# Optimization experiments

Hardware: AMD Instinct MI355X
Metric: run time of the kernel (lower is better)

Reference implementation:

```python
import jax, jax.numpy as jnp
import numpy as np

N, H, S, R, T = 32768, 512, 8, 64, 12

def setup_inputs() -> dict:
    key = jax.random.key(0)
    ks = jax.random.split(key, 7)
    scale = 1.0 / np.sqrt(H)
    return {
        "encodings": jax.random.normal(ks[0], (N, H), dtype=jnp.float32),
        "domain_encs": jax.random.normal(ks[1], (S, H), dtype=jnp.float32),
        "Us": jax.random.normal(ks[2], (S, H, R), dtype=jnp.float32) * scale,
        "W1": jax.random.normal(ks[3], (S, H, H), dtype=jnp.float32) * scale,
        "b1": jax.random.normal(ks[4], (S, H), dtype=jnp.float32) * 0.01,
        "W2": jax.random.normal(ks[5], (S, H, T), dtype=jnp.float32) * scale,
        "b2": jax.random.normal(ks[6], (S, T), dtype=jnp.float32) * 0.01,
    }

def reference(encodings, domain_encs, Us, W1, b1, W2, b2):
    # Mahalanobis soft routing. Original computes (p-mu) @ (U U^T) @ (p-mu)^T
    # and takes sqrt(diag) -- algebraically identical to project-then-square-sum.
    diff = encodings[None, :, :] - domain_encs[:, None, :]        # [S, N, H]
    proj = jnp.einsum('snh,shr->snr', diff, Us)                   # [S, N, R]
    dist = jnp.sqrt(jnp.sum(proj * proj, axis=-1))                # [S, N]
    alphas = jax.nn.softmax(-dist, axis=0)                        # softmax over sources

    # Per-source classifier: Dropout(eval=identity) -> ReLU -> Linear(H,H)
    # -> Dropout -> ReLU -> Linear(H,T) -> Sigmoid
    h0 = jax.nn.relu(encodings)                                   # [N, H]
    h1 = jax.nn.relu(jnp.einsum('nh,shk->snk', h0, W1) + b1[:, None, :])  # [S, N, H]
    out = jax.nn.sigmoid(jnp.einsum('snk,skt->snt', h1, W2) + b2[:, None, :])  # [S, N, T]

    # Softmax-weighted combine of expert outputs
    return jnp.sum(alphas[:, :, None] * out, axis=0)              # [N, T]
```

## Files before the change

kernel.cpp:

```cpp
#include <hip/hip_runtime.h>
#include <hip/hip_bf16.h>

typedef unsigned short u16;
typedef __bf16 bf16x8 __attribute__((ext_vector_type(8)));
typedef float f32x4 __attribute__((ext_vector_type(4)));

#define NROWS 32768
#define H 512
#define NS 8
#define NR 64
#define NT 12

#define WS_W1T   0
#define WS_UCT   4194304
#define WS_W2T   4718592
#define WS_CVEC  4849664
#define WS_ALPH  4851712

union BFU { __bf16 h; u16 u; };
__device__ __forceinline__ u16 f2bf(float v) { BFU b; b.h = (__bf16)v; return b.u; }

__device__ __forceinline__ void gload16(const u16* g, u16* l) {
  __builtin_amdgcn_global_load_lds(
      (const __attribute__((address_space(1))) unsigned int*)g,
      (__attribute__((address_space(3))) unsigned int*)l, 16, 0, 0);
}

__global__ __launch_bounds__(256) void transpose_cast(const float* __restrict__ in,
    u16* __restrict__ out, int Rr, int Cc, int Cpad) {
  __shared__ float tile[32][33];
  int b = blockIdx.z, r0 = blockIdx.x * 32, c0 = blockIdx.y * 32;
  int tx = threadIdx.x, ty = threadIdx.y;
#pragma unroll
  for (int i = 0; i < 4; i++) {
    int r = r0 + ty + i * 8, c = c0 + tx;
    float v = 0.f;
    if (r < Rr && c < Cc) v = in[((size_t)b * Rr + r) * Cc + c];
    tile[ty + i * 8][tx] = v;
  }
  __syncthreads();
#pragma unroll
  for (int i = 0; i < 4; i++) {
    int c = c0 + ty + i * 8, r = r0 + tx;
    if (c < Cpad && r < Rr) out[((size_t)b * Cpad + c) * Rr + r] = f2bf(tile[tx][ty + i * 8]);
  }
}

__global__ __launch_bounds__(64) void compute_c(const float* __restrict__ mu,
                                                const float* __restrict__ Us,
                                                float* __restrict__ cvec) {
  int s = blockIdx.x >> 6, r = blockIdx.x & 63, t = threadIdx.x;
  float acc = 0.f;
#pragma unroll
  for (int k = t; k < H; k += 64) acc += mu[s * H + k] * Us[((size_t)s * H + k) * NR + r];
#pragma unroll
  for (int m = 32; m; m >>= 1) acc += __shfl_xor(acc, m, 64);
  if (t == 0) cvec[blockIdx.x] = acc;
}

__device__ __forceinline__ void stage32r(const u16* __restrict__ g, u16* l, int wave, int lane) {
#pragma unroll
  for (int i = 0; i < 8; i++) {
    int r = wave * 8 + i;
    gload16(g + (size_t)r * 512 + (size_t)((lane ^ (r & 7)) * 8), l + r * 512);
  }
}

__global__ __launch_bounds__(256, 2) void routing(
    const float* __restrict__ enc, const u16* __restrict__ UcatT,
    const float* __restrict__ cvec, float* __restrict__ alphT) {
  __shared__ __align__(16) u16 Wst[2][32 * 512];
  __shared__ float distS[NS][64];

  const int tid = threadIdx.x;
  const int wave = tid >> 6, lane = tid & 63;
  const int lnm = lane & 15, lnq = lane >> 4;
  const int row0 = blockIdx.x * 64;

  bf16x8 afrag[16];
  {
    const float* rp = enc + (size_t)(row0 + wave * 16 + lnm) * H + lnq * 8;
#pragma unroll
    for (int ks = 0; ks < 16; ks++) {
      float4 x0 = *(const float4*)(rp + ks * 32);
      float4 x1 = *(const float4*)(rp + ks * 32 + 4);
      bf16x8 a;
      a[0] = (__bf16)x0.x; a[1] = (__bf16)x0.y; a[2] = (__bf16)x0.z; a[3] = (__bf16)x0.w;
      a[4] = (__bf16)x1.x; a[5] = (__bf16)x1.y; a[6] = (__bf16)x1.z; a[7] = (__bf16)x1.w;
      afrag[ks] = a;
    }
  }

  stage32r(UcatT, Wst[0], wave, lane);
  float dsq[4] = {0.f, 0.f, 0.f, 0.f};
#pragma unroll 1
  for (int q = 0; q < 16; q++) {
    int s = q >> 1, half = q & 1;
    __syncthreads();
    if (q < 15) stage32r(UcatT + (size_t)(q + 1) * 32 * 512, Wst[(q + 1) & 1], wave, lane);
    const u16* buf = Wst[q & 1];
    f32x4 acc[2] = {};
#pragma unroll
    for (int ks = 0; ks < 16; ks++) {
      int uu = ((ks * 4 + lnq) ^ (lnm & 7)) * 8;
      bf16x8 b0 = *(const bf16x8*)&buf[lnm * 512 + uu];
      bf16x8 b1v = *(const bf16x8*)&buf[(16 + lnm) * 512 + uu];
      acc[0] = __builtin_amdgcn_mfma_f32_16x16x32_bf16(afrag[ks], b0, acc[0], 0, 0, 0);
      acc[1] = __builtin_amdgcn_mfma_f32_16x16x32_bf16(afrag[ks], b1v, acc[1], 0, 0, 0);
    }
#pragma unroll
    for (int ct = 0; ct < 2; ct++) {
      float cv = cvec[s * 64 + half * 32 + ct * 16 + lnm];
#pragma unroll
      for (int g = 0; g < 4; g++) { float d = acc[ct][g] - cv; dsq[g] += d * d; }
    }
    if (half == 1) {
#pragma unroll
      for (int m = 1; m < 16; m <<= 1) {
#pragma unroll
        for (int g = 0; g < 4; g++) dsq[g] += __shfl_xor(dsq[g], m, 16);
      }
      if (lnm == 0) {
#pragma unroll
        for (int g = 0; g < 4; g++) distS[s][wave * 16 + lnq * 4 + g] = sqrtf(dsq[g]);
      }
#pragma unroll
      for (int g = 0; g < 4; g++) dsq[g] = 0.f;
    }
  }
  __syncthreads();
  if (tid < 64) {
    float dmin = distS[0][tid];
#pragma unroll
    for (int s = 1; s < NS; s++) dmin = fminf(dmin, distS[s][tid]);
    float den = 0.f, e[NS];
#pragma unroll
    for (int s = 0; s < NS; s++) { e[s] = __expf(dmin - distS[s][tid]); den += e[s]; }
    float inv = 1.f / den;
#pragma unroll
    for (int s = 0; s < NS; s++) alphT[(size_t)s * NROWS + row0 + tid] = e[s] * inv;
  }
}

#define H1STR 40

__device__ __forceinline__ void stageW16(const u16* __restrict__ g, u16* l, int tid) {
#pragma unroll
  for (int i = 0; i < 4; i++) {
    int flat = tid + i * 256;
    int r = flat >> 5, u = flat & 31;
    gload16(g + (size_t)r * 512 + (u ^ (r & 7)) * 8, l + flat * 8);
  }
}

__device__ __forceinline__ const u16* chunk_base(const u16* W1g, int q) {
  return W1g + ((size_t)(q >> 5) * 512 + ((q >> 1) & 15) * 32) * 512 + (q & 1) * 256;
}

__global__ __launch_bounds__(256, 2) void moe_main(
    const float* __restrict__ enc, const u16* __restrict__ W1T,
    const u16* __restrict__ W2T, const float* __restrict__ alphT,
    const float* __restrict__ b1g, const float* __restrict__ b2g,
    float* __restrict__ out) {
  __shared__ __align__(16) u16 Wst[3][32 * 256];
  __shared__ __align__(16) u16 h1c[128 * H1STR];
  __shared__ float alphS[4][128];

  const int tid = threadIdx.x;
  const int wave = tid >> 6, lane = tid & 63;
  const int lnm = lane & 15, lnq = lane >> 4;
  const int rb = blockIdx.x >> 1, sg = blockIdx.x & 1;
  const int row0 = rb * 128, sbase = sg * 4;

#pragma unroll
  for (int i = 0; i < 2; i++) {
    int u = tid + i * 256, j = u >> 7, r = u & 127;
    alphS[j][r] = alphT[(size_t)(sbase + j) * NROWS + row0 + r];
  }

  bf16x8 efrag[2][16];
#pragma unroll
  for (int t = 0; t < 2; t++) {
    const float* rp = enc + (size_t)(row0 + wave * 32 + t * 16 + lnm) * H + lnq * 8;
#pragma unroll
    for (int ks = 0; ks < 16; ks++) {
      float4 x0 = *(const float4*)(rp + ks * 32);
      float4 x1 = *(const float4*)(rp + ks * 32 + 4);
      bf16x8 a;
      a[0] = (__bf16)fmaxf(x0.x, 0.f); a[1] = (__bf16)fmaxf(x0.y, 0.f);
      a[2] = (__bf16)fmaxf(x0.z, 0.f); a[3] = (__bf16)fmaxf(x0.w, 0.f);
      a[4] = (__bf16)fmaxf(x1.x, 0.f); a[5] = (__bf16)fmaxf(x1.y, 0.f);
      a[6] = (__bf16)fmaxf(x1.z, 0.f); a[7] = (__bf16)fmaxf(x1.w, 0.f);
      efrag[t][ks] = a;
    }
  }

  __syncthreads();

  const u16* W1g = W1T + (size_t)sbase * 512 * 512;
  stageW16(chunk_base(W1g, 0), Wst[0], tid);
  int cb = 0;
  f32x4 acc[2][2];
  float fin[2][4] = {};
#pragma unroll 1
  for (int j = 0; j < 4; j++) {
    const int s = sbase + j;
    f32x4 oacc[2] = {};
#pragma unroll 1
    for (int wc = 0; wc < 16; wc++) {
      const int q = j * 32 + wc * 2;
      {
        const int nb = (cb == 2) ? 0 : cb + 1;
        stageW16(chunk_base(W1g, q + 1), Wst[nb], tid);
        asm volatile("s_waitcnt vmcnt(4)" ::: "memory");
        __builtin_amdgcn_s_barrier();
        const u16* buf = Wst[cb];
#pragma unroll
        for (int t = 0; t < 2; t++) { acc[t][0] = (f32x4){0,0,0,0}; acc[t][1] = (f32x4){0,0,0,0}; }
        __builtin_amdgcn_s_setprio(1);
#pragma unroll
        for (int ks = 0; ks < 8; ks++) {
          const int uu = ((ks * 4 + lnq) ^ (lnm & 7)) * 8;
          bf16x8 w0 = *(const bf16x8*)&buf[lnm * 256 + uu];
          bf16x8 w1 = *(const bf16x8*)&buf[(16 + lnm) * 256 + uu];
#pragma unroll
          for (int t = 0; t < 2; t++) {
            acc[t][0] = __builtin_amdgcn_mfma_f32_16x16x32_bf16(w0, efrag[t][ks], acc[t][0], 0, 0, 0);
            acc[t][1] = __builtin_amdgcn_mfma_f32_16x16x32_bf16(w1, efrag[t][ks], acc[t][1], 0, 0, 0);
          }
        }
        __builtin_amdgcn_s_setprio(0);
        cb = nb;
      }
      {
        const int nb = (cb == 2) ? 0 : cb + 1;
        if (q + 2 < 128) {
          stageW16(chunk_base(W1g, q + 2), Wst[nb], tid);
          asm volatile("s_waitcnt vmcnt(4)" ::: "memory");
        } else {
          asm volatile("s_waitcnt vmcnt(0)" ::: "memory");
        }
        __builtin_amdgcn_s_barrier();
        const u16* buf = Wst[cb];
        __builtin_amdgcn_s_setprio(1);
#pragma unroll
        for (int ks = 0; ks < 8; ks++) {
          const int uu = ((ks * 4 + lnq) ^ (lnm & 7)) * 8;
          bf16x8 w0 = *(const bf16x8*)&buf[lnm * 256 + uu];
          bf16x8 w1 = *(const bf16x8*)&buf[(16 + lnm) * 256 + uu];
#pragma unroll
          for (int t = 0; t < 2; t++) {
            acc[t][0] = __builtin_amdgcn_mfma_f32_16x16x32_bf16(w0, efrag[t][8 + ks], acc[t][0], 0, 0, 0);
            acc[t][1] = __builtin_amdgcn_mfma_f32_16x16x32_bf16(w1, efrag[t][8 + ks], acc[t][1], 0, 0, 0);
          }
        }
        __builtin_amdgcn_s_setprio(0);
        cb = nb;
      }
#pragma unroll
      for (int ct = 0; ct < 2; ct++) {
        float4 bq = *(const float4*)&b1g[s * H + wc * 32 + ct * 16 + lnq * 4];
#pragma unroll
        for (int t = 0; t < 2; t++) {
          union { u16 u[4]; uint2 v; } pk;
          pk.u[0] = f2bf(fmaxf(acc[t][ct][0] + bq.x, 0.f));
          pk.u[1] = f2bf(fmaxf(acc[t][ct][1] + bq.y, 0.f));
          pk.u[2] = f2bf(fmaxf(acc[t][ct][2] + bq.z, 0.f));
          pk.u[3] = f2bf(fmaxf(acc[t][ct][3] + bq.w, 0.f));
          *(uint2*)&h1c[(wave * 32 + t * 16 + lnm) * H1STR + ct * 16 + lnq * 4] = pk.v;
        }
      }
      {
        bf16x8 bw = *(const bf16x8*)&W2T[((size_t)s * 16 + lnm) * H + wc * 32 + lnq * 8];
#pragma unroll
        for (int t = 0; t < 2; t++) {
          bf16x8 a2 = *(const bf16x8*)&h1c[(wave * 32 + t * 16 + lnm) * H1STR + lnq * 8];
          oacc[t] = __builtin_amdgcn_mfma_f32_16x16x32_bf16(a2, bw, oacc[t], 0, 0, 0);
        }
      }
    }
    {
      float b2v = (lnm < NT) ? b2g[s * NT + lnm] : 0.f;
#pragma unroll
      for (int t = 0; t < 2; t++) {
#pragma unroll
        for (int g = 0; g < 4; g++) {
          float sig = 1.f / (1.f + __expf(-(oacc[t][g] + b2v)));
          fin[t][g] += alphS[j][wave * 32 + t * 16 + lnq * 4 + g] * sig;
        }
      }
    }
  }
  if (lnm < NT) {
#pragma unroll
    for (int t = 0; t < 2; t++) {
#pragma unroll
      for (int g = 0; g < 4; g++) {
        int rg = row0 + wave * 32 + t * 16 + lnq * 4 + g;
        atomicAdd(&out[(size_t)rg * NT + lnm], fin[t][g]);
      }
    }
  }
}

extern "C" void kernel_launch(void* const* d_in, const int* in_sizes, int n_in,
                              void* d_out, int out_size, void* d_ws, size_t ws_size,
                              hipStream_t stream) {
  const float* enc = (const float*)d_in[0];
  const float* mu  = (const float*)d_in[1];
  const float* Us  = (const float*)d_in[2];
  const float* W1  = (const float*)d_in[3];
  const float* b1  = (const float*)d_in[4];
  const float* W2  = (const float*)d_in[5];
  const float* b2  = (const float*)d_in[6];
  float* out = (float*)d_out;
  char* ws = (char*)d_ws;
  u16* W1T    = (u16*)(ws + WS_W1T);
  u16* UcatT  = (u16*)(ws + WS_UCT);
  u16* W2T    = (u16*)(ws + WS_W2T);
  float* cvec = (float*)(ws + WS_CVEC);
  float* alphT = (float*)(ws + WS_ALPH);

  dim3 tb(32, 8, 1);
  transpose_cast<<<dim3(16, 16, 8), tb, 0, stream>>>(W1, W1T, 512, 512, 512);
  transpose_cast<<<dim3(16, 2, 8),  tb, 0, stream>>>(Us, UcatT, 512, 64, 64);
  transpose_cast<<<dim3(16, 1, 8),  tb, 0, stream>>>(W2, W2T, 512, 12, 16);
  compute_c<<<512, 64, 0, stream>>>(mu, Us, cvec);
  routing<<<512, 256, 0, stream>>>(enc, UcatT, cvec, alphT);
  hipMemsetAsync(out, 0, (size_t)out_size * sizeof(float), stream);
  moe_main<<<512, 256, 0, stream>>>(enc, W1T, W2T, alphT, b1, b2, out);
}
```

Measured before the change: 291.8 us.

## Split W1 tile between LDS staging and direct per-wave register loads

```diff
diff --git a/kernel.cpp b/kernel.cpp
--- a/kernel.cpp
+++ b/kernel.cpp
@@ -144,12 +144,12 @@
 
 #define H1STR 40
 
-__device__ __forceinline__ void stageW16(const u16* __restrict__ g, u16* l, int tid) {
-#pragma unroll
-  for (int i = 0; i < 4; i++) {
+__device__ __forceinline__ void stageW8(const u16* __restrict__ g, u16* l, int tid) {
+#pragma unroll
+  for (int i = 0; i < 2; i++) {
     int flat = tid + i * 256;
     int r = flat >> 5, u = flat & 31;
-    gload16(g + (size_t)r * 512 + (u ^ (r & 7)) * 8, l + flat * 8);
+    gload16(g + (size_t)r * 512 + ((u ^ (r & 7)) * 8), l + flat * 8);
   }
 }
 
@@ -162,7 +162,7 @@
     const u16* __restrict__ W2T, const float* __restrict__ alphT,
     const float* __restrict__ b1g, const float* __restrict__ b2g,
     float* __restrict__ out) {
-  __shared__ __align__(16) u16 Wst[3][32 * 256];
+  __shared__ __align__(16) u16 Wst[3][16 * 256];
   __shared__ __align__(16) u16 h1c[128 * H1STR];
   __shared__ float alphS[4][128];
 
@@ -177,6 +177,10 @@
     int u = tid + i * 256, j = u >> 7, r = u & 127;
     alphS[j][r] = alphT[(size_t)(sbase + j) * NROWS + row0 + r];
   }
+
+  float b2v[4];
+#pragma unroll
+  for (int j = 0; j < 4; j++) b2v[j] = (lnm < NT) ? b2g[(sbase + j) * NT + lnm] : 0.f;
 
   bf16x8 efrag[2][16];
 #pragma unroll
@@ -198,7 +202,7 @@
   __syncthreads();
 
   const u16* W1g = W1T + (size_t)sbase * 512 * 512;
-  stageW16(chunk_base(W1g, 0), Wst[0], tid);
+  stageW8(chunk_base(W1g, 0), Wst[0], tid);
   int cb = 0;
   f32x4 acc[2][2];
   float fin[2][4] = {};
@@ -208,58 +212,48 @@
     f32x4 oacc[2] = {};
 #pragma unroll 1
     for (int wc = 0; wc < 16; wc++) {
-      const int q = j * 32 + wc * 2;
-      {
+      float4 bq0 = *(const float4*)&b1g[s * H + wc * 32 + lnq * 4];
+      float4 bq1 = *(const float4*)&b1g[s * H + wc * 32 + 16 + lnq * 4];
+      bf16x8 bw = *(const bf16x8*)&W2T[((size_t)s * 16 + lnm) * H + wc * 32 + lnq * 8];
+#pragma unroll
+      for (int t = 0; t < 2; t++) { acc[t][0] = (f32x4){0,0,0,0}; acc[t][1] = (f32x4){0,0,0,0}; }
+#pragma unroll
+      for (int kh = 0; kh < 2; kh++) {
+        const int q = j * 32 + wc * 2 + kh;
+        bf16x8 w1r[8];
+        const u16* w1p = W1g + ((size_t)(j * 512 + wc * 32 + 16 + lnm)) * 512 + kh * 256 + lnq * 8;
+#pragma unroll
+        for (int ksl = 0; ksl < 8; ksl++) w1r[ksl] = *(const bf16x8*)(w1p + ksl * 32);
         const int nb = (cb == 2) ? 0 : cb + 1;
-        stageW16(chunk_base(W1g, q + 1), Wst[nb], tid);
-        asm volatile("s_waitcnt vmcnt(4)" ::: "memory");
-        __builtin_amdgcn_s_barrier();
-        const u16* buf = Wst[cb];
-#pragma unroll
-        for (int t = 0; t < 2; t++) { acc[t][0] = (f32x4){0,0,0,0}; acc[t][1] = (f32x4){0,0,0,0}; }
-        __builtin_amdgcn_s_setprio(1);
-#pragma unroll
-        for (int ks = 0; ks < 8; ks++) {
-          const int uu = ((ks * 4 + lnq) ^ (lnm & 7)) * 8;
-          bf16x8 w0 = *(const bf16x8*)&buf[lnm * 256 + uu];
-          bf16x8 w1 = *(const bf16x8*)&buf[(16 + lnm) * 256 + uu];
-#pragma unroll
-          for (int t = 0; t < 2; t++) {
-            acc[t][0] = __builtin_amdgcn_mfma_f32_16x16x32_bf16(w0, efrag[t][ks], acc[t][0], 0, 0, 0);
-            acc[t][1] = __builtin_amdgcn_mfma_f32_16x16x32_bf16(w1, efrag[t][ks], acc[t][1], 0, 0, 0);
-          }
-        }
-        __builtin_amdgcn_s_setprio(0);
-        cb = nb;
-      }
-      {
-        const int nb = (cb == 2) ? 0 : cb + 1;
-        if (q + 2 < 128) {
-          stageW16(chunk_base(W1g, q + 2), Wst[nb], tid);
-          asm volatile("s_waitcnt vmcnt(4)" ::: "memory");
+        if (q + 1 < 128) {
+          stageW8(chunk_base(W1g, q + 1), Wst[nb], tid);
+          asm volatile("s_waitcnt vmcnt(10)" ::: "memory");
         } else {
-          asm volatile("s_waitcnt vmcnt(0)" ::: "memory");
+          asm volatile("s_waitcnt vmcnt(8)" ::: "memory");
         }
         __builtin_amdgcn_s_barrier();
         const u16* buf = Wst[cb];
         __builtin_amdgcn_s_setprio(1);
 #pragma unroll
-        for (int ks = 0; ks < 8; ks++) {
-          const int uu = ((ks * 4 + lnq) ^ (lnm & 7)) * 8;
+        for (int ksl = 0; ksl < 8; ksl++) {
+          const int uu = ((ksl * 4 + lnq) ^ (lnm & 7)) * 8;
           bf16x8 w0 = *(const bf16x8*)&buf[lnm * 256 + uu];
-          bf16x8 w1 = *(const bf16x8*)&buf[(16 + lnm) * 256 + uu];
-#pragma unroll
-          for (int t = 0; t < 2; t++) {
-            acc[t][0] = __builtin_amdgcn_mfma_f32_16x16x32_bf16(w0, efrag[t][8 + ks], acc[t][0], 0, 0, 0);
-            acc[t][1] = __builtin_amdgcn_mfma_f32_16x16x32_bf16(w1, efrag[t][8 + ks], acc[t][1], 0, 0, 0);
-          }
+#pragma unroll
+          for (int t = 0; t < 2; t++)
+            acc[t][0] = __builtin_amdgcn_mfma_f32_16x16x32_bf16(w0, efrag[t][kh * 8 + ksl], acc[t][0], 0, 0, 0);
+        }
+#pragma unroll
+        for (int ksl = 0; ksl < 8; ksl++) {
+#pragma unroll
+          for (int t = 0; t < 2; t++)
+            acc[t][1] = __builtin_amdgcn_mfma_f32_16x16x32_bf16(w1r[ksl], efrag[t][kh * 8 + ksl], acc[t][1], 0, 0, 0);
         }
         __builtin_amdgcn_s_setprio(0);
         cb = nb;
       }
 #pragma unroll
       for (int ct = 0; ct < 2; ct++) {
-        float4 bq = *(const float4*)&b1g[s * H + wc * 32 + ct * 16 + lnq * 4];
+        float4 bq = ct ? bq1 : bq0;
 #pragma unroll
         for (int t = 0; t < 2; t++) {
           union { u16 u[4]; uint2 v; } pk;
@@ -271,7 +265,6 @@
         }
       }
       {
-        bf16x8 bw = *(const bf16x8*)&W2T[((size_t)s * 16 + lnm) * H + wc * 32 + lnq * 8];
 #pragma unroll
         for (int t = 0; t < 2; t++) {
           bf16x8 a2 = *(const bf16x8*)&h1c[(wave * 32 + t * 16 + lnm) * H1STR + lnq * 8];
@@ -280,12 +273,11 @@
       }
     }
     {
-      float b2v = (lnm < NT) ? b2g[s * NT + lnm] : 0.f;
 #pragma unroll
       for (int t = 0; t < 2; t++) {
 #pragma unroll
         for (int g = 0; g < 4; g++) {
-          float sig = 1.f / (1.f + __expf(-(oacc[t][g] + b2v)));
+          float sig = 1.f / (1.f + __expf(-(oacc[t][g] + b2v[j])));
           fin[t][g] += alphS[j][wave * 32 + t * 16 + lnq * 4 + g] * sig;
         }
       }
```

Result: slower. 426.9 us (+46.3%).

## Double routing rows per block with triple-buffered staging; hoist bias/W2 loads in moe_main

Applied to the files above, without the earlier changes.

```diff
diff --git a/kernel.cpp b/kernel.cpp
--- a/kernel.cpp
+++ b/kernel.cpp
@@ -58,28 +58,34 @@
   if (t == 0) cvec[blockIdx.x] = acc;
 }
 
-__device__ __forceinline__ void stage32r(const u16* __restrict__ g, u16* l, int wave, int lane) {
-#pragma unroll
-  for (int i = 0; i < 8; i++) {
-    int r = wave * 8 + i;
-    gload16(g + (size_t)r * 512 + (size_t)((lane ^ (r & 7)) * 8), l + r * 512);
+__device__ __forceinline__ void stageW16(const u16* __restrict__ g, u16* l, int tid) {
+#pragma unroll
+  for (int i = 0; i < 4; i++) {
+    int flat = tid + i * 256;
+    int r = flat >> 5, u = flat & 31;
+    gload16(g + (size_t)r * 512 + (u ^ (r & 7)) * 8, l + flat * 8);
   }
 }
 
 __global__ __launch_bounds__(256, 2) void routing(
     const float* __restrict__ enc, const u16* __restrict__ UcatT,
     const float* __restrict__ cvec, float* __restrict__ alphT) {
-  __shared__ __align__(16) u16 Wst[2][32 * 512];
-  __shared__ float distS[NS][64];
+  __shared__ __align__(16) u16 Wst[3][32 * 256];
+  __shared__ float distS[NS][128];
+  __shared__ float cvS[512];
 
   const int tid = threadIdx.x;
   const int wave = tid >> 6, lane = tid & 63;
   const int lnm = lane & 15, lnq = lane >> 4;
-  const int row0 = blockIdx.x * 64;
-
-  bf16x8 afrag[16];
-  {
-    const float* rp = enc + (size_t)(row0 + wave * 16 + lnm) * H + lnq * 8;
+  const int row0 = blockIdx.x * 128;
+
+  cvS[tid] = cvec[tid];
+  cvS[256 + tid] = cvec[256 + tid];
+
+  bf16x8 afrag[2][16];
+#pragma unroll
+  for (int t = 0; t < 2; t++) {
+    const float* rp = enc + (size_t)(row0 + wave * 32 + t * 16 + lnm) * H + lnq * 8;
 #pragma unroll
     for (int ks = 0; ks < 16; ks++) {
       float4 x0 = *(const float4*)(rp + ks * 32);
@@ -87,49 +93,78 @@
       bf16x8 a;
       a[0] = (__bf16)x0.x; a[1] = (__bf16)x0.y; a[2] = (__bf16)x0.z; a[3] = (__bf16)x0.w;
       a[4] = (__bf16)x1.x; a[5] = (__bf16)x1.y; a[6] = (__bf16)x1.z; a[7] = (__bf16)x1.w;
-      afrag[ks] = a;
-    }
-  }
-
-  stage32r(UcatT, Wst[0], wave, lane);
-  float dsq[4] = {0.f, 0.f, 0.f, 0.f};
+      afrag[t][ks] = a;
+    }
+  }
+
+  __syncthreads();
+
+  stageW16(UcatT, Wst[0], tid);
+  int cb = 0;
+  f32x4 acc[2][2];
+  float dsq[2][4] = {};
 #pragma unroll 1
-  for (int q = 0; q < 16; q++) {
-    int s = q >> 1, half = q & 1;
-    __syncthreads();
-    if (q < 15) stage32r(UcatT + (size_t)(q + 1) * 32 * 512, Wst[(q + 1) & 1], wave, lane);
-    const u16* buf = Wst[q & 1];
-    f32x4 acc[2] = {};
-#pragma unroll
-    for (int ks = 0; ks < 16; ks++) {
-      int uu = ((ks * 4 + lnq) ^ (lnm & 7)) * 8;
-      bf16x8 b0 = *(const bf16x8*)&buf[lnm * 512 + uu];
-      bf16x8 b1v = *(const bf16x8*)&buf[(16 + lnm) * 512 + uu];
-      acc[0] = __builtin_amdgcn_mfma_f32_16x16x32_bf16(afrag[ks], b0, acc[0], 0, 0, 0);
-      acc[1] = __builtin_amdgcn_mfma_f32_16x16x32_bf16(afrag[ks], b1v, acc[1], 0, 0, 0);
+  for (int wc = 0; wc < 16; wc++) {
+#pragma unroll
+    for (int t = 0; t < 2; t++) { acc[t][0] = (f32x4){0,0,0,0}; acc[t][1] = (f32x4){0,0,0,0}; }
+#pragma unroll
+    for (int kh = 0; kh < 2; kh++) {
+      const int q = wc * 2 + kh;
+      const int nb = (cb == 2) ? 0 : cb + 1;
+      if (q + 1 < 32) {
+        stageW16(UcatT + (size_t)((q + 1) >> 1) * 32 * 512 + ((q + 1) & 1) * 256, Wst[nb], tid);
+        asm volatile("s_waitcnt vmcnt(4)" ::: "memory");
+      } else {
+        asm volatile("s_waitcnt vmcnt(0)" ::: "memory");
+      }
+      __builtin_amdgcn_s_barrier();
+      const u16* buf = Wst[cb];
+      __builtin_amdgcn_s_setprio(1);
+#pragma unroll
+      for (int ksl = 0; ksl < 8; ksl++) {
+        const int uu = ((ksl * 4 + lnq) ^ (lnm & 7)) * 8;
+        bf16x8 b0 = *(const bf16x8*)&buf[lnm * 256 + uu];
+        bf16x8 b1v = *(const bf16x8*)&buf[(16 + lnm) * 256 + uu];
+#pragma unroll
+        for (int t = 0; t < 2; t++) {
+          acc[t][0] = __builtin_amdgcn_mfma_f32_16x16x32_bf16(afrag[t][kh * 8 + ksl], b0, acc[t][0], 0, 0, 0);
+          acc[t][1] = __builtin_amdgcn_mfma_f32_16x16x32_bf16(afrag[t][kh * 8 + ksl], b1v, acc[t][1], 0, 0, 0);
+        }
+      }
+      __builtin_amdgcn_s_setprio(0);
+      cb = nb;
     }
 #pragma unroll
     for (int ct = 0; ct < 2; ct++) {
-      float cv = cvec[s * 64 + half * 32 + ct * 16 + lnm];
-#pragma unroll
-      for (int g = 0; g < 4; g++) { float d = acc[ct][g] - cv; dsq[g] += d * d; }
-    }
-    if (half == 1) {
+      float cv = cvS[wc * 32 + ct * 16 + lnm];
+#pragma unroll
+      for (int t = 0; t < 2; t++)
+#pragma unroll
+        for (int g = 0; g < 4; g++) { float d = acc[t][ct][g] - cv; dsq[t][g] += d * d; }
+    }
+    if (wc & 1) {
 #pragma unroll
       for (int m = 1; m < 16; m <<= 1) {
 #pragma unroll
-        for (int g = 0; g < 4; g++) dsq[g] += __shfl_xor(dsq[g], m, 16);
+        for (int t = 0; t < 2; t++)
+#pragma unroll
+          for (int g = 0; g < 4; g++) dsq[t][g] += __shfl_xor(dsq[t][g], m, 16);
       }
       if (lnm == 0) {
 #pragma unroll
-        for (int g = 0; g < 4; g++) distS[s][wave * 16 + lnq * 4 + g] = sqrtf(dsq[g]);
-      }
-#pragma unroll
-      for (int g = 0; g < 4; g++) dsq[g] = 0.f;
+        for (int t = 0; t < 2; t++)
+#pragma unroll
+          for (int g = 0; g < 4; g++)
+            distS[wc >> 1][wave * 32 + t * 16 + lnq * 4 + g] = sqrtf(dsq[t][g]);
+      }
+#pragma unroll
+      for (int t = 0; t < 2; t++)
+#pragma unroll
+        for (int g = 0; g < 4; g++) dsq[t][g] = 0.f;
     }
   }
   __syncthreads();
-  if (tid < 64) {
+  if (tid < 128) {
     float dmin = distS[0][tid];
 #pragma unroll
     for (int s = 1; s < NS; s++) dmin = fminf(dmin, distS[s][tid]);
@@ -143,15 +178,6 @@
 }
 
 #define H1STR 40
-
-__device__ __forceinline__ void stageW16(const u16* __restrict__ g, u16* l, int tid) {
-#pragma unroll
-  for (int i = 0; i < 4; i++) {
-    int flat = tid + i * 256;
-    int r = flat >> 5, u = flat & 31;
-    gload16(g + (size_t)r * 512 + (u ^ (r & 7)) * 8, l + flat * 8);
-  }
-}
 
 __device__ __forceinline__ const u16* chunk_base(const u16* W1g, int q) {
   return W1g + ((size_t)(q >> 5) * 512 + ((q >> 1) & 15) * 32) * 512 + (q & 1) * 256;
@@ -177,6 +203,10 @@
     int u = tid + i * 256, j = u >> 7, r = u & 127;
     alphS[j][r] = alphT[(size_t)(sbase + j) * NROWS + row0 + r];
   }
+
+  float b2v[4];
+#pragma unroll
+  for (int j = 0; j < 4; j++) b2v[j] = (lnm < NT) ? b2g[(sbase + j) * NT + lnm] : 0.f;
 
   bf16x8 efrag[2][16];
 #pragma unroll
@@ -209,10 +239,14 @@
 #pragma unroll 1
     for (int wc = 0; wc < 16; wc++) {
       const int q = j * 32 + wc * 2;
+      float4 bq0 = *(const float4*)&b1g[s * H + wc * 32 + lnq * 4];
+      float4 bq1 = *(const float4*)&b1g[s * H + wc * 32 + 16 + lnq * 4];
+      bf16x8 bw = *(const bf16x8*)&W2T[((size_t)s * 16 + lnm) * H + wc * 32 + lnq * 8];
+      asm volatile("" ::: "memory");
       {
         const int nb = (cb == 2) ? 0 : cb + 1;
         stageW16(chunk_base(W1g, q + 1), Wst[nb], tid);
-        asm volatile("s_waitcnt vmcnt(4)" ::: "memory");
+        asm volatile("s_waitcnt vmcnt(7)" ::: "memory");
         __builtin_amdgcn_s_barrier();
         const u16* buf = Wst[cb];
 #pragma unroll
@@ -259,7 +293,7 @@
       }
 #pragma unroll
       for (int ct = 0; ct < 2; ct++) {
-        float4 bq = *(const float4*)&b1g[s * H + wc * 32 + ct * 16 + lnq * 4];
+        float4 bq = ct ? bq1 : bq0;
 #pragma unroll
         for (int t = 0; t < 2; t++) {
           union { u16 u[4]; uint2 v; } pk;
@@ -271,7 +305,6 @@
         }
       }
       {
-        bf16x8 bw = *(const bf16x8*)&W2T[((size_t)s * 16 + lnm) * H + wc * 32 + lnq * 8];
 #pragma unroll
         for (int t = 0; t < 2; t++) {
           bf16x8 a2 = *(const bf16x8*)&h1c[(wave * 32 + t * 16 + lnm) * H1STR + lnq * 8];
@@ -280,12 +313,11 @@
       }
     }
     {
-      float b2v = (lnm < NT) ? b2g[s * NT + lnm] : 0.f;
 #pragma unroll
       for (int t = 0; t < 2; t++) {
 #pragma unroll
         for (int g = 0; g < 4; g++) {
-          float sig = 1.f / (1.f + __expf(-(oacc[t][g] + b2v)));
+          float sig = 1.f / (1.f + __expf(-(oacc[t][g] + b2v[j])));
           fin[t][g] += alphS[j][wave * 32 + t * 16 + lnq * 4 + g] * sig;
         }
       }
@@ -326,7 +358,7 @@
   transpose_cast<<<dim3(16, 2, 8),  tb, 0, stream>>>(Us, UcatT, 512, 64, 64);
   transpose_cast<<<dim3(16, 1, 8),  tb, 0, stream>>>(W2, W2T, 512, 12, 16);
   compute_c<<<512, 64, 0, stream>>>(mu, Us, cvec);
-  routing<<<512, 256, 0, stream>>>(enc, UcatT, cvec, alphT);
+  routing<<<256, 256, 0, stream>>>(enc, UcatT, cvec, alphT);
   hipMemsetAsync(out, 0, (size_t)out_size * sizeof(float), stream);
   moe_main<<<512, 256, 0, stream>>>(enc, W1T, W2T, alphT, b1, b2, out);
 }
```

Result: no change. 289.6 us (-0.8%).
